# Optimization experiments

Hardware: AMD Instinct MI355X
Metric: run time of the kernel (lower is better)

Reference implementation:

```python
import jax, jax.numpy as jnp
import numpy as np

DIM = 3072
NUM_HEADS = 24
HEAD_DIM = DIM // NUM_HEADS  # 128
SEQ = 2048
BATCH = 1


def rms_norm(x, scale):
    # compute in fp32 like the torch module
    xf = x.astype(jnp.float32)
    rrms = jax.lax.rsqrt(jnp.mean(xf * xf, axis=-1, keepdims=True) + 1e-6)
    return (xf * rrms).astype(x.dtype) * scale


def apply_rope(xq, xk, pe):
    # xq, xk: [B, H, L, D]; pe: [B, 1, L, D//2, 2, 2]
    shp = xq.shape
    xq_ = xq.reshape(*shp[:-1], -1, 1, 2).astype(jnp.float32)
    xk_ = xk.reshape(*shp[:-1], -1, 1, 2).astype(jnp.float32)
    xq_out = pe[..., 0] * xq_[..., 0] + pe[..., 1] * xq_[..., 1]
    xk_out = pe[..., 0] * xk_[..., 0] + pe[..., 1] * xk_[..., 1]
    return xq_out.reshape(shp).astype(xq.dtype), xk_out.reshape(shp).astype(xk.dtype)


def setup_inputs() -> dict:
    key = jax.random.key(0)
    ks = jax.random.split(key, 6)
    s = 1.0 / np.sqrt(DIM)
    return {
        "x": jax.random.normal(ks[0], (BATCH, SEQ, DIM), dtype=jnp.float32),
        "pe": jax.random.normal(ks[1], (BATCH, 1, SEQ, HEAD_DIM // 2, 2, 2), dtype=jnp.float32),
        "w_qkv": jax.random.normal(ks[2], (3 * DIM, DIM), dtype=jnp.float32) * s,
        "w_proj": jax.random.normal(ks[3], (DIM, DIM), dtype=jnp.float32) * s,
        "b_proj": jax.random.normal(ks[4], (DIM,), dtype=jnp.float32) * 0.01,
        "q_scale": jnp.ones((HEAD_DIM,), dtype=jnp.float32),
        "k_scale": jnp.ones((HEAD_DIM,), dtype=jnp.float32),
    }


def reference(x, pe, w_qkv, w_proj, b_proj, q_scale, k_scale):
    B, L, _ = x.shape
    # fused qkv projection (qkv_bias=False)
    qkv = jnp.einsum("bld,ed->ble", x, w_qkv)  # [B, L, 3*DIM]
    qkv = qkv.reshape(B, L, 3, NUM_HEADS, HEAD_DIM)
    qkv = jnp.transpose(qkv, (2, 0, 3, 1, 4))  # [3, B, H, L, D]
    q, k, v = qkv[0], qkv[1], qkv[2]
    # QKNorm (RMSNorm on head_dim)
    q = rms_norm(q, q_scale).astype(v.dtype)
    k = rms_norm(k, k_scale).astype(v.dtype)
    # rope
    q, k = apply_rope(q, k, pe)
    # scaled dot-product attention
    scale = 1.0 / np.sqrt(HEAD_DIM)
    scores = jnp.einsum("bhqd,bhkd->bhqk", q, k) * scale
    probs = jax.nn.softmax(scores, axis=-1)
    out = jnp.einsum("bhqk,bhkd->bhqd", probs, v)
    out = jnp.transpose(out, (0, 2, 1, 3)).reshape(B, L, DIM)  # merge heads
    # output projection
    return jnp.einsum("bld,ed->ble", out, w_proj) + b_proj
```

## Files before the change

### kernel.cpp

```cpp
#include <hip/hip_runtime.h>

typedef __bf16 bf16;
typedef __attribute__((ext_vector_type(8))) __bf16 bf16x8;
typedef __attribute__((ext_vector_type(4))) float f32x4;

typedef __attribute__((address_space(1))) void gvoid_t;
typedef __attribute__((address_space(3))) void lvoid_t;

#define LDS_LOAD16(gp, lp) \
    __builtin_amdgcn_global_load_lds((gvoid_t*)(gp), (lvoid_t*)(lp), 16, 0, 0)

__global__ __launch_bounds__(256)
void f32_to_bf16(const float* __restrict__ in, bf16* __restrict__ out, int n8)
{
    const int i = blockIdx.x * 256 + threadIdx.x;
    if (i >= n8) return;
    const float4 a = ((const float4*)in)[i * 2];
    const float4 b = ((const float4*)in)[i * 2 + 1];
    bf16x8 o;
    o[0] = (bf16)a.x; o[1] = (bf16)a.y; o[2] = (bf16)a.z; o[3] = (bf16)a.w;
    o[4] = (bf16)b.x; o[5] = (bf16)b.y; o[6] = (bf16)b.z; o[7] = (bf16)b.w;
    *(bf16x8*)(out + (size_t)i * 8) = o;
}

template <int BIAS, typename CT>
__global__ __launch_bounds__(256, 2)
void gemm_bt(const bf16* __restrict__ A, const bf16* __restrict__ B,
             const float* __restrict__ bias, CT* __restrict__ C,
             int K, int ldc)
{
    __shared__ bf16 sA[128 * 32];
    __shared__ bf16 sB[128 * 32];
    const int tid  = threadIdx.x;
    const int lane = tid & 63;
    const int wid  = tid >> 6;
    const int m0 = blockIdx.y * 128;
    const int n0 = blockIdx.x * 128;
    const int wm = (wid >> 1) * 64;
    const int wn = (wid & 1) * 64;
    const int l15   = lane & 15;
    const int quad8 = (lane >> 4) * 8;

    f32x4 acc[4][4] = {};

    for (int k0 = 0; k0 < K; k0 += 32) {
#pragma unroll
        for (int t = 0; t < 2; ++t) {
            const int e  = (t * 4 + wid) * 512;
            const int ge = e + lane * 8;
            const int r = ge >> 5, c = ge & 31;
            LDS_LOAD16(A + (size_t)(m0 + r) * K + k0 + c, sA + e);
            LDS_LOAD16(B + (size_t)(n0 + r) * K + k0 + c, sB + e);
        }
        __syncthreads();

        bf16x8 af[4], bfr[4];
#pragma unroll
        for (int i = 0; i < 4; ++i) {
            af[i]  = *(const bf16x8*)(sA + (wm + i * 16 + l15) * 32 + quad8);
            bfr[i] = *(const bf16x8*)(sB + (wn + i * 16 + l15) * 32 + quad8);
        }
#pragma unroll
        for (int i = 0; i < 4; ++i)
#pragma unroll
            for (int j = 0; j < 4; ++j)
                acc[i][j] = __builtin_amdgcn_mfma_f32_16x16x32_bf16(af[i], bfr[j], acc[i][j], 0, 0, 0);
        __syncthreads();
    }

    const int rowBase = m0 + wm + (lane >> 4) * 4;
    const int colBase = n0 + wn + l15;
#pragma unroll
    for (int j = 0; j < 4; ++j) {
        const int col = colBase + j * 16;
        const float bv = BIAS ? bias[col] : 0.0f;
#pragma unroll
        for (int i = 0; i < 4; ++i) {
            const int row = rowBase + i * 16;
#pragma unroll
            for (int r = 0; r < 4; ++r)
                C[(size_t)(row + r) * ldc + col] = (CT)(acc[i][j][r] + bv);
        }
    }
}

template <int BIAS, typename CT>
__global__ __launch_bounds__(512, 4)
void gemm128_bt(const bf16* __restrict__ A, const bf16* __restrict__ B,
                const float* __restrict__ bias, CT* __restrict__ C,
                int K, int ldc)
{
    __shared__ bf16 sA[2 * 128 * 64];
    __shared__ bf16 sB[2 * 192 * 64];

    const int tid  = threadIdx.x;
    const int lane = tid & 63;
    const int wid  = tid >> 6;
    const int m0 = blockIdx.y * 128;
    const int n0 = blockIdx.x * 192;
    const int wm = (wid >> 2) * 64;
    const int wn = (wid & 3) * 48;
    const int l15  = lane & 15;
    const int quad = lane >> 4;

    int aoff[2], boff[3];
    int adst[2], bdst[3];
#pragma unroll
    for (int t = 0; t < 2; ++t) {
        const int slot = t * 512 + tid;
        const int r  = slot >> 3;
        const int cg = (slot & 7) ^ (r & 7);
        aoff[t] = (m0 + r) * K + cg * 8;
        adst[t] = (t * 512 + wid * 64) * 8;
    }
#pragma unroll
    for (int t = 0; t < 3; ++t) {
        const int slot = t * 512 + tid;
        const int r  = slot >> 3;
        const int cg = (slot & 7) ^ (r & 7);
        boff[t] = (n0 + r) * K + cg * 8;
        bdst[t] = (t * 512 + wid * 64) * 8;
    }

#define STA(t, kt, buf) LDS_LOAD16(A + (size_t)aoff[t] + (kt) * 64, sA + (buf) * 8192  + adst[t])
#define STB(t, kt, buf) LDS_LOAD16(B + (size_t)boff[t] + (kt) * 64, sB + (buf) * 12288 + bdst[t])

    int aRd[2], bRd[2];
#pragma unroll
    for (int kk = 0; kk < 2; ++kk) {
        const int pcg = (kk * 4 + quad) ^ (l15 & 7);
        aRd[kk] = (wm + l15) * 128 + pcg * 16;
        bRd[kk] = (wn + l15) * 128 + pcg * 16;
    }

    f32x4 acc[4][3] = {};

#pragma unroll
    for (int t = 0; t < 2; ++t) STA(t, 0, 0);
#pragma unroll
    for (int t = 0; t < 3; ++t) STB(t, 0, 0);
    asm volatile("s_waitcnt vmcnt(0)" ::: "memory");

    const int NT = K >> 6;
#pragma unroll 1
    for (int u = 0; u < NT; ++u) {
        const int b = u & 1;
        __builtin_amdgcn_s_barrier();
        if (u + 1 < NT) {
            STA(0, u + 1, b ^ 1); STA(1, u + 1, b ^ 1);
            STB(0, u + 1, b ^ 1); STB(1, u + 1, b ^ 1); STB(2, u + 1, b ^ 1);
        }
        __builtin_amdgcn_sched_barrier(0);

        bf16x8 af[4][2], bfr[3][2];
#pragma unroll
        for (int mi = 0; mi < 2; ++mi)
#pragma unroll
            for (int kk = 0; kk < 2; ++kk)
                af[mi][kk] = *(const bf16x8*)((const char*)sA + b * 16384 +
                                              aRd[kk] + mi * 2048);
#pragma unroll
        for (int nf = 0; nf < 3; ++nf)
#pragma unroll
            for (int kk = 0; kk < 2; ++kk)
                bfr[nf][kk] = *(const bf16x8*)((const char*)sB + b * 24576 +
                                               bRd[kk] + nf * 2048);
        __builtin_amdgcn_sched_barrier(0);
#pragma unroll
        for (int mi = 2; mi < 4; ++mi)
#pragma unroll
            for (int kk = 0; kk < 2; ++kk)
                af[mi][kk] = *(const bf16x8*)((const char*)sA + b * 16384 +
                                              aRd[kk] + mi * 2048);
        __builtin_amdgcn_sched_barrier(0);

        asm volatile("s_waitcnt lgkmcnt(4)" ::: "memory");
        __builtin_amdgcn_sched_barrier(0);
        __builtin_amdgcn_s_setprio(1);
#pragma unroll
        for (int mi = 0; mi < 2; ++mi)
#pragma unroll
            for (int nf = 0; nf < 3; ++nf)
#pragma unroll
                for (int kk = 0; kk < 2; ++kk)
                    acc[mi][nf] = __builtin_amdgcn_mfma_f32_16x16x32_bf16(
                        af[mi][kk], bfr[nf][kk], acc[mi][nf], 0, 0, 0);
        __builtin_amdgcn_sched_barrier(0);
        asm volatile("s_waitcnt lgkmcnt(0)" ::: "memory");
        __builtin_amdgcn_sched_barrier(0);
#pragma unroll
        for (int mi = 2; mi < 4; ++mi)
#pragma unroll
            for (int nf = 0; nf < 3; ++nf)
#pragma unroll
                for (int kk = 0; kk < 2; ++kk)
                    acc[mi][nf] = __builtin_amdgcn_mfma_f32_16x16x32_bf16(
                        af[mi][kk], bfr[nf][kk], acc[mi][nf], 0, 0, 0);
        __builtin_amdgcn_s_setprio(0);
        __builtin_amdgcn_sched_barrier(0);
        asm volatile("s_waitcnt vmcnt(0)" ::: "memory");
    }
#undef STA
#undef STB

    const int rowBase = m0 + wm + quad * 4;
    const int colBase = n0 + wn + l15;
#pragma unroll
    for (int nf = 0; nf < 3; ++nf) {
        const int col = colBase + nf * 16;
        const float bv = BIAS ? bias[col] : 0.0f;
#pragma unroll
        for (int mf = 0; mf < 4; ++mf) {
            const int row = rowBase + mf * 16;
#pragma unroll
            for (int r = 0; r < 4; ++r)
                C[(size_t)(row + r) * ldc + col] = (CT)(acc[mf][nf][r] + bv);
        }
    }
}

__global__ __launch_bounds__(256)
void qk_rope_rearrange(const bf16* __restrict__ qkv, const float* __restrict__ pe,
                       const float* __restrict__ qs, const float* __restrict__ ks,
                       bf16* __restrict__ Qh, bf16* __restrict__ Kh, bf16* __restrict__ Vt)
{
    const int lane = threadIdx.x & 63;
    const int wid  = threadIdx.x >> 6;
    const int idx  = blockIdx.x * 4 + wid;
    const int h = idx >> 11;
    const int l = idx & 2047;

    const size_t rowb = (size_t)l * 9216 + h * 128 + 2 * lane;
    const float q0 = (float)qkv[rowb];
    const float q1 = (float)qkv[rowb + 1];
    const float k0 = (float)qkv[rowb + 3072];
    const float k1 = (float)qkv[rowb + 3073];
    const bf16  v0 = qkv[rowb + 6144];
    const bf16  v1 = qkv[rowb + 6145];

    float ssq = q0 * q0 + q1 * q1;
    float ssk = k0 * k0 + k1 * k1;
#pragma unroll
    for (int off = 1; off < 64; off <<= 1) {
        ssq += __shfl_xor(ssq, off);
        ssk += __shfl_xor(ssk, off);
    }
    const float rq = rsqrtf(ssq * (1.0f / 128.0f) + 1e-6f);
    const float rk = rsqrtf(ssk * (1.0f / 128.0f) + 1e-6f);

    const float s0q = qs[2 * lane], s1q = qs[2 * lane + 1];
    const float s0k = ks[2 * lane], s1k = ks[2 * lane + 1];

    const float qn0 = (q0 * rq) * s0q;
    const float qn1 = (q1 * rq) * s1q;
    const float kn0 = (k0 * rk) * s0k;
    const float kn1 = (k1 * rk) * s1k;

    const float* pp = pe + ((size_t)l * 64 + lane) * 4;
    const float p00 = pp[0], p01 = pp[1];
    const float p10 = pp[2], p11 = pp[3];

    const bf16 qo0 = (bf16)(p00 * qn0 + p01 * qn1);
    const bf16 qo1 = (bf16)(p10 * qn0 + p11 * qn1);
    const bf16 ko0 = (bf16)(p00 * kn0 + p01 * kn1);
    const bf16 ko1 = (bf16)(p10 * kn0 + p11 * kn1);

    const size_t ob = ((size_t)h * 2048 + l) * 128 + 2 * lane;
    Qh[ob] = qo0; Qh[ob + 1] = qo1;
    Kh[ob] = ko0; Kh[ob + 1] = ko1;

    const size_t vb = ((size_t)h * 128 + 2 * lane) * 2048 + l;
    Vt[vb]        = v0;
    Vt[vb + 2048] = v1;
}

__global__ __launch_bounds__(256, 2)
void flash_attn(const bf16* __restrict__ Qh, const bf16* __restrict__ Kh,
                const bf16* __restrict__ Vt, bf16* __restrict__ AO)
{
    __shared__ bf16 sK[2 * 64 * 128];
    __shared__ bf16 sV[2 * 128 * 64];
    __shared__ bf16 sP[4 * 16 * 72];

    const int tid   = threadIdx.x;
    const int lane  = tid & 63;
    const int wid   = tid >> 6;
    const int h     = blockIdx.y;
    const int qw    = blockIdx.x * 64 + wid * 16;
    const int l15   = lane & 15;
    const int quad  = lane >> 4;
    const int quad8 = quad * 8;

    const bf16* Kbase = Kh + (size_t)h * 2048 * 128;
    const bf16* Vbase = Vt + (size_t)h * 128 * 2048;

    bf16x8 aq[4];
    {
        const bf16* qp = Qh + ((size_t)h * 2048 + qw + l15) * 128 + quad8;
#pragma unroll
        for (int ki = 0; ki < 4; ++ki) aq[ki] = *(const bf16x8*)(qp + ki * 32);
    }

    bf16x8 ones;
#pragma unroll
    for (int i = 0; i < 8; ++i) ones[i] = (bf16)1.0f;

    f32x4 o[8] = {};
    f32x4 lacc = {};

    bf16* sPw = sP + wid * (16 * 72);
    const int slotbase = wid * 64;

#define STAGE_K(kv, buf)                                                         \
    {                                                                            \
        bf16* kb = sK + (buf) * (64 * 128);                                      \
        _Pragma("unroll")                                                        \
        for (int t = 0; t < 4; ++t) {                                            \
            const int sb   = t * 256 + slotbase;                                 \
            const int slot = sb + lane;                                          \
            const int r    = slot >> 4;                                          \
            const int cg   = (slot & 15) ^ (r & 7);                              \
            LDS_LOAD16(Kbase + (size_t)((kv) + r) * 128 + cg * 8, kb + sb * 8);  \
        }                                                                        \
    }
#define STAGE_V(kv, buf)                                                         \
    {                                                                            \
        bf16* vb = sV + (buf) * (128 * 64);                                      \
        _Pragma("unroll")                                                        \
        for (int t = 0; t < 4; ++t) {                                            \
            const int sb   = t * 256 + slotbase;                                 \
            const int slot = sb + lane;                                          \
            const int r    = slot >> 3;                                          \
            const int cg   = (slot & 7) ^ (r & 7);                               \
            LDS_LOAD16(Vbase + (size_t)r * 2048 + (kv) + cg * 8, vb + sb * 8);   \
        }                                                                        \
    }

    STAGE_K(0, 0);
    STAGE_V(0, 0);

    for (int s = 0; s < 32; ++s) {
        __syncthreads();
        if (s < 31) {
            STAGE_K((s + 1) * 64, (s + 1) & 1);
            STAGE_V((s + 1) * 64, (s + 1) & 1);
        }

        const bf16* kb = sK + (s & 1) * (64 * 128);
        const bf16* vb = sV + (s & 1) * (128 * 64);

        f32x4 sc[4];
#pragma unroll
        for (int nt = 0; nt < 4; ++nt) {
            f32x4 t = {};
            const int row = nt * 16 + l15;
#pragma unroll
            for (int ki = 0; ki < 4; ++ki) {
                const int pcg = (4 * ki + quad) ^ (l15 & 7);
                bf16x8 bk = *(const bf16x8*)(kb + row * 128 + pcg * 8);
                t = __builtin_amdgcn_mfma_f32_16x16x32_bf16(aq[ki], bk, t, 0, 0, 0);
            }
            sc[nt] = t;
        }

#pragma unroll
        for (int r = 0; r < 4; ++r) {
            const float scl = 0.08838834764831845f;
            bf16* pw = sPw + (quad * 4 + r) * 72 + l15;
            pw[0]  = (bf16)__expf(sc[0][r] * scl);
            pw[16] = (bf16)__expf(sc[1][r] * scl);
            pw[32] = (bf16)__expf(sc[2][r] * scl);
            pw[48] = (bf16)__expf(sc[3][r] * scl);
        }

#pragma unroll
        for (int kk = 0; kk < 2; ++kk) {
            bf16x8 pa = *(const bf16x8*)(sPw + l15 * 72 + kk * 32 + quad8);
            lacc = __builtin_amdgcn_mfma_f32_16x16x32_bf16(pa, ones, lacc, 0, 0, 0);
#pragma unroll
            for (int dt = 0; dt < 8; ++dt) {
                const int row = dt * 16 + l15;
                const int pcg = (kk * 4 + quad) ^ (l15 & 7);
                bf16x8 bv = *(const bf16x8*)(vb + row * 64 + pcg * 8);
                o[dt] = __builtin_amdgcn_mfma_f32_16x16x32_bf16(pa, bv, o[dt], 0, 0, 0);
            }
        }
    }
#undef STAGE_K
#undef STAGE_V

#pragma unroll
    for (int r = 0; r < 4; ++r) {
        const float inv = 1.0f / lacc[r];
        const size_t row = qw + quad * 4 + r;
        bf16* op = AO + row * 3072 + h * 128 + l15;
#pragma unroll
        for (int dt = 0; dt < 8; ++dt) op[dt * 16] = (bf16)(o[dt][r] * inv);
    }
}

extern "C" void kernel_launch(void* const* d_in, const int* in_sizes, int n_in,
                              void* d_out, int out_size, void* d_ws, size_t ws_size,
                              hipStream_t stream)
{
    (void)in_sizes; (void)n_in; (void)out_size;

    const float* x      = (const float*)d_in[0];
    const float* pe     = (const float*)d_in[1];
    const float* w_qkv  = (const float*)d_in[2];
    const float* w_proj = (const float*)d_in[3];
    const float* b_proj = (const float*)d_in[4];
    const float* q_s    = (const float*)d_in[5];
    const float* k_s    = (const float*)d_in[6];
    float* out = (float*)d_out;

    const size_t NEED_BIG = ((size_t)6291456 + 28311552 + 18874368 + 6291456) * 2;

    if (ws_size >= NEED_BIG) {
        bf16* xb  = (bf16*)d_ws;
        bf16* wb  = xb + (size_t)6291456;
        bf16* qkv = wb + (size_t)28311552;
        bf16* Vt  = qkv + (size_t)18874368;
        bf16* Qh  = xb;
        bf16* Kh  = wb;
        bf16* wpb = qkv;
        bf16* AO  = qkv + (size_t)9437184;

        f32_to_bf16<<<dim3(3072),  256, 0, stream>>>(x,     xb, 786432);
        f32_to_bf16<<<dim3(13824), 256, 0, stream>>>(w_qkv, wb, 3538944);
        gemm128_bt<0, bf16><<<dim3(48, 16), 512, 0, stream>>>(xb, wb, nullptr, qkv, 3072, 9216);
        qk_rope_rearrange<<<dim3(12288), 256, 0, stream>>>(qkv, pe, q_s, k_s, Qh, Kh, Vt);
        f32_to_bf16<<<dim3(4608), 256, 0, stream>>>(w_proj, wpb, 1179648);
        flash_attn<<<dim3(32, 24), 256, 0, stream>>>(Qh, Kh, Vt, AO);
        gemm_bt<1, float><<<dim3(24, 16), 256, 0, stream>>>(AO, wpb, b_proj, out, 3072, 3072);
    } else {
        bf16* xb  = (bf16*)d_ws;
        bf16* wb  = xb + (size_t)6291456;
        bf16* qkv = wb + (size_t)9437184;
        bf16* Vt  = qkv + (size_t)18874368;
        bf16* Qh  = xb;
        bf16* Kh  = wb;
        bf16* wpb = qkv;
        bf16* AO  = qkv + (size_t)9437184;

        f32_to_bf16<<<dim3(3072), 256, 0, stream>>>(x, xb, 786432);
        for (int c = 0; c < 3; ++c) {
            f32_to_bf16<<<dim3(4608), 256, 0, stream>>>(w_qkv + (size_t)c * 9437184, wb, 1179648);
            gemm_bt<0, bf16><<<dim3(24, 16), 256, 0, stream>>>(xb, wb, nullptr, qkv + c * 3072, 3072, 9216);
        }
        qk_rope_rearrange<<<dim3(12288), 256, 0, stream>>>(qkv, pe, q_s, k_s, Qh, Kh, Vt);
        f32_to_bf16<<<dim3(4608), 256, 0, stream>>>(w_proj, wpb, 1179648);
        flash_attn<<<dim3(32, 24), 256, 0, stream>>>(Qh, Kh, Vt, AO);
        gemm_bt<1, float><<<dim3(24, 16), 256, 0, stream>>>(AO, wpb, b_proj, out, 3072, 3072);
    }
}
```

Measured before the change: 555.4 us.

## Add 64x192-tile output projection GEMM and raise MFMA priority in attention

Adds a new gemm64_bt kernel with 64x192 tiles, 512 threads and double-buffered LDS staging through direct global-to-LDS loads. It replaces the older gemm_bt for the output projection, raising the block count from 384 to 512 so more of the GPU's compute units are busy. The flash-attention loop also wraps its MFMA sections in s_setprio so matrix work gets issue priority over the other waves. The smaller M tile reuses each loaded B tile across fewer rows, which raises global traffic per FLOP.

Result: faster. 535.3 us (-3.6%).

```diff
diff --git a/kernel.cpp b/kernel.cpp
--- a/kernel.cpp
+++ b/kernel.cpp
@@ -219,6 +219,129 @@
     }
 }
 
+template <int BIAS, typename CT>
+__global__ __launch_bounds__(512, 4)
+void gemm64_bt(const bf16* __restrict__ A, const bf16* __restrict__ B,
+               const float* __restrict__ bias, CT* __restrict__ C,
+               int K, int ldc)
+{
+    __shared__ bf16 sA[2 * 64 * 64];
+    __shared__ bf16 sB[2 * 192 * 64];
+
+    const int tid  = threadIdx.x;
+    const int lane = tid & 63;
+    const int wid  = tid >> 6;
+    const int m0 = blockIdx.y * 64;
+    const int n0 = blockIdx.x * 192;
+    const int wm = (wid >> 2) * 32;
+    const int wn = (wid & 3) * 48;
+    const int l15  = lane & 15;
+    const int quad = lane >> 4;
+
+    int aoff, adst;
+    {
+        const int slot = tid;
+        const int r  = slot >> 3;
+        const int cg = (slot & 7) ^ (r & 7);
+        aoff = (m0 + r) * K + cg * 8;
+        adst = (wid * 64) * 8;
+    }
+    int boff[3], bdst[3];
+#pragma unroll
+    for (int t = 0; t < 3; ++t) {
+        const int slot = t * 512 + tid;
+        const int r  = slot >> 3;
+        const int cg = (slot & 7) ^ (r & 7);
+        boff[t] = (n0 + r) * K + cg * 8;
+        bdst[t] = (t * 512 + wid * 64) * 8;
+    }
+
+#define STA64(kt, buf)    LDS_LOAD16(A + (size_t)aoff    + (kt) * 64, sA + (buf) * 4096  + adst)
+#define STB64(t, kt, buf) LDS_LOAD16(B + (size_t)boff[t] + (kt) * 64, sB + (buf) * 12288 + bdst[t])
+
+    int aRd[2], bRd[2];
+#pragma unroll
+    for (int kk = 0; kk < 2; ++kk) {
+        const int pcg = (kk * 4 + quad) ^ (l15 & 7);
+        aRd[kk] = (wm + l15) * 128 + pcg * 16;
+        bRd[kk] = (wn + l15) * 128 + pcg * 16;
+    }
+
+    f32x4 acc[2][3] = {};
+
+    STA64(0, 0);
+#pragma unroll
+    for (int t = 0; t < 3; ++t) STB64(t, 0, 0);
+    asm volatile("s_waitcnt vmcnt(0)" ::: "memory");
+
+    const int NT = K >> 6;
+#pragma unroll 1
+    for (int u = 0; u < NT; ++u) {
+        const int b = u & 1;
+        __builtin_amdgcn_s_barrier();
+        if (u + 1 < NT) {
+            STA64(u + 1, b ^ 1);
+            STB64(0, u + 1, b ^ 1); STB64(1, u + 1, b ^ 1); STB64(2, u + 1, b ^ 1);
+        }
+        __builtin_amdgcn_sched_barrier(0);
+
+        bf16x8 af[2][2], bfr[3][2];
+#pragma unroll
+        for (int kk = 0; kk < 2; ++kk)
+            af[0][kk] = *(const bf16x8*)((const char*)sA + b * 8192 + aRd[kk]);
+#pragma unroll
+        for (int nf = 0; nf < 3; ++nf)
+#pragma unroll
+            for (int kk = 0; kk < 2; ++kk)
+                bfr[nf][kk] = *(const bf16x8*)((const char*)sB + b * 24576 +
+                                               bRd[kk] + nf * 2048);
+        __builtin_amdgcn_sched_barrier(0);
+#pragma unroll
+        for (int kk = 0; kk < 2; ++kk)
+            af[1][kk] = *(const bf16x8*)((const char*)sA + b * 8192 + aRd[kk] + 2048);
+        __builtin_amdgcn_sched_barrier(0);
+
+        asm volatile("s_waitcnt lgkmcnt(2)" ::: "memory");
+        __builtin_amdgcn_sched_barrier(0);
+        __builtin_amdgcn_s_setprio(1);
+#pragma unroll
+        for (int nf = 0; nf < 3; ++nf)
+#pragma unroll
+            for (int kk = 0; kk < 2; ++kk)
+                acc[0][nf] = __builtin_amdgcn_mfma_f32_16x16x32_bf16(
+                    af[0][kk], bfr[nf][kk], acc[0][nf], 0, 0, 0);
+        __builtin_amdgcn_sched_barrier(0);
+        asm volatile("s_waitcnt lgkmcnt(0)" ::: "memory");
+        __builtin_amdgcn_sched_barrier(0);
+#pragma unroll
+        for (int nf = 0; nf < 3; ++nf)
+#pragma unroll
+            for (int kk = 0; kk < 2; ++kk)
+                acc[1][nf] = __builtin_amdgcn_mfma_f32_16x16x32_bf16(
+                    af[1][kk], bfr[nf][kk], acc[1][nf], 0, 0, 0);
+        __builtin_amdgcn_s_setprio(0);
+        __builtin_amdgcn_sched_barrier(0);
+        asm volatile("s_waitcnt vmcnt(0)" ::: "memory");
+    }
+#undef STA64
+#undef STB64
+
+    const int rowBase = m0 + wm + quad * 4;
+    const int colBase = n0 + wn + l15;
+#pragma unroll
+    for (int nf = 0; nf < 3; ++nf) {
+        const int col = colBase + nf * 16;
+        const float bv = BIAS ? bias[col] : 0.0f;
+#pragma unroll
+        for (int mf = 0; mf < 2; ++mf) {
+            const int row = rowBase + mf * 16;
+#pragma unroll
+            for (int r = 0; r < 4; ++r)
+                C[(size_t)(row + r) * ldc + col] = (CT)(acc[mf][nf][r] + bv);
+        }
+    }
+}
+
 __global__ __launch_bounds__(256)
 void qk_rope_rearrange(const bf16* __restrict__ qkv, const float* __restrict__ pe,
                        const float* __restrict__ qs, const float* __restrict__ ks,
@@ -350,6 +473,7 @@
         const bf16* vb = sV + (s & 1) * (128 * 64);
 
         f32x4 sc[4];
+        __builtin_amdgcn_s_setprio(1);
 #pragma unroll
         for (int nt = 0; nt < 4; ++nt) {
             f32x4 t = {};
@@ -362,6 +486,7 @@
             }
             sc[nt] = t;
         }
+        __builtin_amdgcn_s_setprio(0);
 
 #pragma unroll
         for (int r = 0; r < 4; ++r) {
@@ -373,6 +498,7 @@
             pw[48] = (bf16)__expf(sc[3][r] * scl);
         }
 
+        __builtin_amdgcn_s_setprio(1);
 #pragma unroll
         for (int kk = 0; kk < 2; ++kk) {
             bf16x8 pa = *(const bf16x8*)(sPw + l15 * 72 + kk * 32 + quad8);
@@ -385,6 +511,7 @@
                 o[dt] = __builtin_amdgcn_mfma_f32_16x16x32_bf16(pa, bv, o[dt], 0, 0, 0);
             }
         }
+        __builtin_amdgcn_s_setprio(0);
     }
 #undef STAGE_K
 #undef STAGE_V
@@ -432,7 +559,7 @@
         qk_rope_rearrange<<<dim3(12288), 256, 0, stream>>>(qkv, pe, q_s, k_s, Qh, Kh, Vt);
         f32_to_bf16<<<dim3(4608), 256, 0, stream>>>(w_proj, wpb, 1179648);
         flash_attn<<<dim3(32, 24), 256, 0, stream>>>(Qh, Kh, Vt, AO);
-        gemm_bt<1, float><<<dim3(24, 16), 256, 0, stream>>>(AO, wpb, b_proj, out, 3072, 3072);
+        gemm64_bt<1, float><<<dim3(16, 32), 512, 0, stream>>>(AO, wpb, b_proj, out, 3072, 3072);
     } else {
         bf16* xb  = (bf16*)d_ws;
         bf16* wb  = xb + (size_t)6291456;
@@ -451,6 +578,6 @@
         qk_rope_rearrange<<<dim3(12288), 256, 0, stream>>>(qkv, pe, q_s, k_s, Qh, Kh, Vt);
         f32_to_bf16<<<dim3(4608), 256, 0, stream>>>(w_proj, wpb, 1179648);
         flash_attn<<<dim3(32, 24), 256, 0, stream>>>(Qh, Kh, Vt, AO);
-        gemm_bt<1, float><<<dim3(24, 16), 256, 0, stream>>>(AO, wpb, b_proj, out, 3072, 3072);
-    }
-}
+        gemm64_bt<1, float><<<dim3(16, 32), 512, 0, stream>>>(AO, wpb, b_proj, out, 3072, 3072);
+    }
+}
```
